# Kernel tuning notes

Hardware: AMD Instinct MI355X
Metric: run time of the kernel (lower is better)

Reference implementation:

```python
import jax, jax.numpy as jnp
import numpy as np

N = 10000
K1, K2 = 10, 25
DIM = 64
OUT = 128
NUM_GRAPHS = 64


def setup_inputs() -> dict:
    key = jax.random.key(0)
    ks = jax.random.split(key, 10)
    h0 = jax.random.normal(ks[0], (N, DIM), jnp.float32)
    h1 = jax.random.normal(ks[1], (N * K1, DIM), jnp.float32)
    h2 = jax.random.normal(ks[2], (N * K1 * K2, DIM), jnp.float32)
    # glorot-ish scaled weights
    w0 = jax.random.normal(ks[3], (2 * DIM, OUT), jnp.float32) * (2.0 / (2 * DIM + OUT)) ** 0.5
    b0 = jnp.zeros((OUT,), jnp.float32)
    w1 = jax.random.normal(ks[4], (2 * OUT, OUT), jnp.float32) * (2.0 / (3 * OUT)) ** 0.5
    b1 = jnp.zeros((OUT,), jnp.float32)
    wr1 = jax.random.normal(ks[5], (OUT, 35), jnp.float32) * (2.0 / (OUT + 35)) ** 0.5
    br1 = jnp.zeros((35,), jnp.float32)
    wr2 = jax.random.normal(ks[6], (35, 35), jnp.float32) * (2.0 / 70) ** 0.5
    br2 = jnp.zeros((35,), jnp.float32)
    wr3 = jax.random.normal(ks[7], (35, 1), jnp.float32) * (2.0 / 36) ** 0.5
    br3 = jnp.zeros((1,), jnp.float32)
    states_graph_ids = jnp.sort(jax.random.randint(ks[8], (N,), 0, NUM_GRAPHS, jnp.int32))
    return {
        "h0": h0, "h1": h1, "h2": h2,
        "w0": w0, "b0": b0, "w1": w1, "b1": b1,
        "wr1": wr1, "br1": br1, "wr2": wr2, "br2": br2, "wr3": wr3, "br3": br3,
        "states_graph_ids": states_graph_ids, "num_graphs": NUM_GRAPHS,
    }


def _aggr_mean(src, neigh, w, b):
    # GraphSAGE mean aggregator: concat(src, mean(neighbors)) @ w + b, relu
    n, d = src.shape
    k = neigh.shape[0] // n
    neigh_mean = neigh.reshape(n, k, d).mean(axis=1)  # (n, d)
    return jax.nn.relu(jnp.concatenate([src, neigh_mean], axis=1) @ w + b)


def reference(h0, h1, h2, w0, b0, w1, b1, wr1, br1, wr2, br2, wr3, br3,
              states_graph_ids, num_graphs):
    # round 0: shared aggregator across depths
    a01 = _aggr_mean(h0, h1, w0, b0)          # (N, OUT)
    a12 = _aggr_mean(h1, h2, w0, b0)          # (N*K1, OUT)
    # round 1
    out = _aggr_mean(a01, a12, w1, b1)        # (N, OUT)
    # segment_sum over sorted graph ids
    seg = jax.ops.segment_sum(out, states_graph_ids, num_segments=num_graphs,
                              indices_are_sorted=True)  # (G, OUT)
    # readout MLP (dropout inactive at inference)
    r = jax.nn.selu(seg @ wr1 + br1)
    r = jax.nn.selu(r @ wr2 + br2)
    r = r @ wr3 + br3                          # (G, 1)
    return r
```

## Files before the change

kernel.cpp:

```cpp
#include <hip/hip_runtime.h>
#include <math.h>

#define N_NODES 10000
#define K1 10
#define K2 25
#define DIM 64
#define OUT 128
#define NGRAPH 64

#define NPB 2
#define RPB (NPB * K1)
#define XROWS (RPB + NPB)
#define QP 36
#define XPITCH (4 * QP)
#define QP1 68
#define X1PITCH (4 * QP1)

__global__ __launch_bounds__(256, 4) void kFused(
    const float* __restrict__ h0, const float* __restrict__ h1,
    const float* __restrict__ h2, const float* __restrict__ w0,
    const float* __restrict__ b0, const float* __restrict__ w1,
    const float* __restrict__ b1, const int* __restrict__ gids,
    float* __restrict__ seg)
{
    __shared__ float xbuf[XROWS][XPITCH];
    __shared__ float x1p[NPB][X1PITCH];

    const int t  = threadIdx.x;
    const int w  = t >> 6;
    const int l  = t & 63;
    const int kq = l & 3;
    const int cp = l >> 2;
    const int c0 = w * 32 + cp * 2;
    const int n0 = blockIdx.x * NPB;

    float w0r0[32], w0r1[32];
#pragma unroll
    for (int kk = 0; kk < 32; ++kk) {
        w0r0[kk] = w0[(kq * 32 + kk) * OUT + c0];
        w0r1[kk] = w0[(kq * 32 + kk) * OUT + c0 + 1];
    }
    const float b00 = b0[c0], b01 = b0[c0 + 1];

    if (t < NPB * DIM) {
        const int i = t >> 6, cl = t & 63;
        xbuf[RPB + i][(cl >> 5) * QP + (cl & 31)] = h0[(size_t)(n0 + i) * DIM + cl];
    }

#pragma unroll 1
    for (int q = 0; q < 5; ++q) {
        const int rloc = w + 4 * q;
        const size_t rg = (size_t)n0 * K1 + rloc;
        const float* hb = h2 + rg * (size_t)(K2 * DIM) + l;
        float s = 0.f;
#pragma unroll
        for (int row = 0; row < K2; ++row)
            s += __builtin_nontemporal_load(hb + row * DIM);
        xbuf[rloc][(2 + (l >> 5)) * QP + (l & 31)] = s * (1.f / K2);
        xbuf[rloc][(l >> 5) * QP + (l & 31)]       = h1[rg * DIM + l];
    }
    __syncthreads();

    if (t < NPB * DIM) {
        const int i = t >> 6, cl = t & 63;
        float s = 0.f;
#pragma unroll
        for (int j = 0; j < K1; ++j)
            s += xbuf[i * K1 + j][(cl >> 5) * QP + (cl & 31)];
        xbuf[RPB + i][(2 + (cl >> 5)) * QP + (cl & 31)] = s * (1.f / K1);
    }
    __syncthreads();

    float accA0 = 0.f, accA1 = 0.f, accB0 = 0.f, accB1 = 0.f;
#pragma unroll 2
    for (int j = 0; j < XROWS; ++j) {
        const float4* xq = (const float4*)&xbuf[j][kq * QP];
        float p0 = 0.f, p1 = 0.f;
#pragma unroll
        for (int m = 0; m < 8; ++m) {
            const float4 x4 = xq[m];
            p0 += x4.x * w0r0[4*m]   + x4.y * w0r0[4*m+1]
                + x4.z * w0r0[4*m+2] + x4.w * w0r0[4*m+3];
            p1 += x4.x * w0r1[4*m]   + x4.y * w0r1[4*m+1]
                + x4.z * w0r1[4*m+2] + x4.w * w0r1[4*m+3];
        }
        p0 += __shfl_xor(p0, 1);  p0 += __shfl_xor(p0, 2);
        p1 += __shfl_xor(p1, 1);  p1 += __shfl_xor(p1, 2);
        const float y0 = fmaxf(p0 + b00, 0.f);
        const float y1 = fmaxf(p1 + b01, 0.f);
        if (j < K1)        { accA0 += y0; accA1 += y1; }
        else if (j < RPB)  { accB0 += y0; accB1 += y1; }
        else if (kq == 0) {
            const int i = j - RPB;
            float2* dst = (float2*)&x1p[i][(c0 >> 6) * QP1 + (c0 & 63)];
            *dst = make_float2(y0, y1);
        }
    }
    if (kq == 0) {
        const int C = OUT + c0;
        float2* d0 = (float2*)&x1p[0][(C >> 6) * QP1 + (C & 63)];
        *d0 = make_float2(accA0 * (1.f / K1), accA1 * (1.f / K1));
        float2* d1 = (float2*)&x1p[1][(C >> 6) * QP1 + (C & 63)];
        *d1 = make_float2(accB0 * (1.f / K1), accB1 * (1.f / K1));
    }
    __syncthreads();

    float pr00 = 0.f, pr01 = 0.f, pr10 = 0.f, pr11 = 0.f;
#pragma unroll 1
    for (int hh = 0; hh < 2; ++hh) {
        float w1r0[32], w1r1[32];
#pragma unroll
        for (int kk = 0; kk < 32; ++kk) {
            const int krow = kq * 64 + hh * 32 + kk;
            w1r0[kk] = w1[krow * OUT + c0];
            w1r1[kk] = w1[krow * OUT + c0 + 1];
        }
        {
            const float4* xq = (const float4*)&x1p[0][kq * QP1 + hh * 32];
            float p0 = 0.f, p1 = 0.f;
#pragma unroll
            for (int m = 0; m < 8; ++m) {
                const float4 x4 = xq[m];
                p0 += x4.x*w1r0[4*m] + x4.y*w1r0[4*m+1] + x4.z*w1r0[4*m+2] + x4.w*w1r0[4*m+3];
                p1 += x4.x*w1r1[4*m] + x4.y*w1r1[4*m+1] + x4.z*w1r1[4*m+2] + x4.w*w1r1[4*m+3];
            }
            pr00 += p0; pr01 += p1;
        }
        {
            const float4* xq = (const float4*)&x1p[1][kq * QP1 + hh * 32];
            float p0 = 0.f, p1 = 0.f;
#pragma unroll
            for (int m = 0; m < 8; ++m) {
                const float4 x4 = xq[m];
                p0 += x4.x*w1r0[4*m] + x4.y*w1r0[4*m+1] + x4.z*w1r0[4*m+2] + x4.w*w1r0[4*m+3];
                p1 += x4.x*w1r1[4*m] + x4.y*w1r1[4*m+1] + x4.z*w1r1[4*m+2] + x4.w*w1r1[4*m+3];
            }
            pr10 += p0; pr11 += p1;
        }
    }
    const float b10 = b1[c0], b11 = b1[c0 + 1];
    pr00 += __shfl_xor(pr00, 1); pr00 += __shfl_xor(pr00, 2);
    pr01 += __shfl_xor(pr01, 1); pr01 += __shfl_xor(pr01, 2);
    pr10 += __shfl_xor(pr10, 1); pr10 += __shfl_xor(pr10, 2);
    pr11 += __shfl_xor(pr11, 1); pr11 += __shfl_xor(pr11, 2);
    const float o00 = fmaxf(pr00 + b10, 0.f);
    const float o01 = fmaxf(pr01 + b11, 0.f);
    const float o10 = fmaxf(pr10 + b10, 0.f);
    const float o11 = fmaxf(pr11 + b11, 0.f);

    if (kq == 0) {
        const int g0 = gids[n0], g1 = gids[n0 + 1];
        if (g0 == g1) {
            atomicAdd(&seg[g0 * OUT + c0],     o00 + o10);
            atomicAdd(&seg[g0 * OUT + c0 + 1], o01 + o11);
        } else {
            atomicAdd(&seg[g0 * OUT + c0],     o00);
            atomicAdd(&seg[g0 * OUT + c0 + 1], o01);
            atomicAdd(&seg[g1 * OUT + c0],     o10);
            atomicAdd(&seg[g1 * OUT + c0 + 1], o11);
        }
    }
}

__global__ void kC(const float* __restrict__ seg,
                   const float* __restrict__ wr1, const float* __restrict__ br1,
                   const float* __restrict__ wr2, const float* __restrict__ br2,
                   const float* __restrict__ wr3, const float* __restrict__ br3,
                   float* __restrict__ out)
{
    __shared__ float r1[35], r2[35];
    const int g = blockIdx.x, l = threadIdx.x;
    const float* s = seg + (size_t)g * OUT;
    const float SCALE = 1.0507009873554805f;
    const float ALPHA = 1.6732632423543772f;

    if (l < 35) {
        float d = br1[l];
        for (int k = 0; k < OUT; ++k) d += s[k] * wr1[k * 35 + l];
        r1[l] = d > 0.f ? SCALE * d : SCALE * ALPHA * (expf(d) - 1.f);
    }
    __syncthreads();
    if (l < 35) {
        float d = br2[l];
        for (int k = 0; k < 35; ++k) d += r1[k] * wr2[k * 35 + l];
        r2[l] = d > 0.f ? SCALE * d : SCALE * ALPHA * (expf(d) - 1.f);
    }
    __syncthreads();
    if (l == 0) {
        float d = br3[0];
        for (int k = 0; k < 35; ++k) d += r2[k] * wr3[k];
        out[g] = d;
    }
}

extern "C" void kernel_launch(void* const* d_in, const int* in_sizes, int n_in,
                              void* d_out, int out_size, void* d_ws, size_t ws_size,
                              hipStream_t stream)
{
    const float* h0  = (const float*)d_in[0];
    const float* h1  = (const float*)d_in[1];
    const float* h2  = (const float*)d_in[2];
    const float* w0  = (const float*)d_in[3];
    const float* b0  = (const float*)d_in[4];
    const float* w1  = (const float*)d_in[5];
    const float* b1  = (const float*)d_in[6];
    const float* wr1 = (const float*)d_in[7];
    const float* br1 = (const float*)d_in[8];
    const float* wr2 = (const float*)d_in[9];
    const float* br2 = (const float*)d_in[10];
    const float* wr3 = (const float*)d_in[11];
    const float* br3 = (const float*)d_in[12];
    const int*  gids = (const int*)d_in[13];

    float* seg = (float*)d_ws;
    float* out = (float*)d_out;

    hipMemsetAsync(seg, 0, NGRAPH * OUT * sizeof(float), stream);
    kFused<<<N_NODES / NPB, 256, 0, stream>>>(h0, h1, h2, w0, b0, w1, b1, gids, seg);
    kC<<<NGRAPH, 64, 0, stream>>>(seg, wr1, br1, wr2, br2, wr3, br3, out);
}
```

Measured before the change: 1.005 ms.

## Restructure fused SAGE kernel with per-column threads, float4 loads and shared-memory k-split

Thread mapping changes from 4-way k-split with shuffle reductions to one output column per thread, with a 2-way k-split whose halves are combined through shared memory. h2 neighbor sums now use float4 loads spread over row groups with cross-lane shuffles, and h1 and h0 are staged with coalesced float4 copies. The w0 load moves after the h2 streaming. Register pressure (64-element weight arrays plus 22 partials) may rise under the 256x4 launch bound, and the non-temporal loads on h2 are dropped.

```diff
diff --git a/kernel.cpp b/kernel.cpp
--- a/kernel.cpp
+++ b/kernel.cpp
@@ -11,10 +11,6 @@
 #define NPB 2
 #define RPB (NPB * K1)
 #define XROWS (RPB + NPB)
-#define QP 36
-#define XPITCH (4 * QP)
-#define QP1 68
-#define X1PITCH (4 * QP1)
 
 __global__ __launch_bounds__(256, 4) void kFused(
     const float* __restrict__ h0, const float* __restrict__ h1,
@@ -23,141 +19,143 @@
     const float* __restrict__ b1, const int* __restrict__ gids,
     float* __restrict__ seg)
 {
-    __shared__ float xbuf[XROWS][XPITCH];
-    __shared__ float x1p[NPB][X1PITCH];
+    __shared__ float xbuf[XROWS][2 * DIM];
+    __shared__ float pbuf[XROWS][OUT];
+    __shared__ float x1[NPB][2 * OUT];
 
     const int t  = threadIdx.x;
     const int w  = t >> 6;
     const int l  = t & 63;
-    const int kq = l & 3;
-    const int cp = l >> 2;
-    const int c0 = w * 32 + cp * 2;
+    const int c  = t & 127;
+    const int h  = t >> 7;
     const int n0 = blockIdx.x * NPB;
 
-    float w0r0[32], w0r1[32];
-#pragma unroll
-    for (int kk = 0; kk < 32; ++kk) {
-        w0r0[kk] = w0[(kq * 32 + kk) * OUT + c0];
-        w0r1[kk] = w0[(kq * 32 + kk) * OUT + c0 + 1];
-    }
-    const float b00 = b0[c0], b01 = b0[c0 + 1];
-
-    if (t < NPB * DIM) {
-        const int i = t >> 6, cl = t & 63;
-        xbuf[RPB + i][(cl >> 5) * QP + (cl & 31)] = h0[(size_t)(n0 + i) * DIM + cl];
-    }
-
+    {
+        const float4* src = (const float4*)(h1 + (size_t)n0 * (K1 * DIM));
+        float4 v = src[t];
+        *(float4*)&xbuf[t >> 4][4 * (t & 15)] = v;
+        if (t < 64) {
+            float4 v2 = src[256 + t];
+            *(float4*)&xbuf[16 + (t >> 4)][4 * (t & 15)] = v2;
+        }
+        if (t < 32) {
+            const float4* s0 = (const float4*)(h0 + (size_t)n0 * DIM);
+            *(float4*)&xbuf[RPB + (t >> 4)][4 * (t & 15)] = s0[t];
+        }
+    }
+
+    {
+        const int fc  = l & 15;
+        const int rg4 = l >> 4;
 #pragma unroll 1
-    for (int q = 0; q < 5; ++q) {
-        const int rloc = w + 4 * q;
-        const size_t rg = (size_t)n0 * K1 + rloc;
-        const float* hb = h2 + rg * (size_t)(K2 * DIM) + l;
-        float s = 0.f;
-#pragma unroll
-        for (int row = 0; row < K2; ++row)
-            s += __builtin_nontemporal_load(hb + row * DIM);
-        xbuf[rloc][(2 + (l >> 5)) * QP + (l & 31)] = s * (1.f / K2);
-        xbuf[rloc][(l >> 5) * QP + (l & 31)]       = h1[rg * DIM + l];
-    }
-    __syncthreads();
+        for (int q = 0; q < 5; ++q) {
+            const int rloc = w + 4 * q;
+            const size_t rg = (size_t)n0 * K1 + rloc;
+            const float4* hb = (const float4*)h2 + rg * (K2 * DIM / 4);
+            float4 s = make_float4(0.f, 0.f, 0.f, 0.f);
+#pragma unroll
+            for (int k = 0; k < 6; ++k) {
+                const float4 v = hb[(4 * k + rg4) * 16 + fc];
+                s.x += v.x; s.y += v.y; s.z += v.z; s.w += v.w;
+            }
+            if (rg4 == 0) {
+                const float4 v = hb[24 * 16 + fc];
+                s.x += v.x; s.y += v.y; s.z += v.z; s.w += v.w;
+            }
+            s.x += __shfl_xor(s.x, 16); s.y += __shfl_xor(s.y, 16);
+            s.z += __shfl_xor(s.z, 16); s.w += __shfl_xor(s.w, 16);
+            s.x += __shfl_xor(s.x, 32); s.y += __shfl_xor(s.y, 32);
+            s.z += __shfl_xor(s.z, 32); s.w += __shfl_xor(s.w, 32);
+            if (rg4 == 0) {
+                *(float4*)&xbuf[rloc][DIM + 4 * fc] =
+                    make_float4(s.x * (1.f / K2), s.y * (1.f / K2),
+                                s.z * (1.f / K2), s.w * (1.f / K2));
+            }
+        }
+    }
+    __syncthreads();
+
+    float w0r[64];
+#pragma unroll
+    for (int k = 0; k < 64; ++k)
+        w0r[k] = w0[(h * 64 + k) * OUT + c];
+    const float b0r = b0[c];
 
     if (t < NPB * DIM) {
         const int i = t >> 6, cl = t & 63;
         float s = 0.f;
 #pragma unroll
         for (int j = 0; j < K1; ++j)
-            s += xbuf[i * K1 + j][(cl >> 5) * QP + (cl & 31)];
-        xbuf[RPB + i][(2 + (cl >> 5)) * QP + (cl & 31)] = s * (1.f / K1);
-    }
-    __syncthreads();
-
-    float accA0 = 0.f, accA1 = 0.f, accB0 = 0.f, accB1 = 0.f;
-#pragma unroll 2
+            s += xbuf[i * K1 + j][cl];
+        xbuf[RPB + i][DIM + cl] = s * (1.f / K1);
+    }
+    __syncthreads();
+
+    float myp[XROWS];
+#pragma unroll
     for (int j = 0; j < XROWS; ++j) {
-        const float4* xq = (const float4*)&xbuf[j][kq * QP];
+        const float4* xj = (const float4*)(&xbuf[j][h * DIM]);
+        float p = 0.f;
+#pragma unroll
+        for (int k4 = 0; k4 < 16; ++k4) {
+            const float4 xv = xj[k4];
+            p += xv.x * w0r[4 * k4 + 0] + xv.y * w0r[4 * k4 + 1]
+               + xv.z * w0r[4 * k4 + 2] + xv.w * w0r[4 * k4 + 3];
+        }
+        if (h == 1) pbuf[j][c] = p;
+        else        myp[j]     = p;
+    }
+    __syncthreads();
+    if (h == 0) {
+        float accA = 0.f, accB = 0.f;
+#pragma unroll
+        for (int j = 0; j < RPB; ++j) {
+            float y = myp[j] + pbuf[j][c] + b0r;
+            y = fmaxf(y, 0.f);
+            if (j < K1) accA += y; else accB += y;
+        }
+        const float y0 = fmaxf(myp[RPB]     + pbuf[RPB][c]     + b0r, 0.f);
+        const float y1 = fmaxf(myp[RPB + 1] + pbuf[RPB + 1][c] + b0r, 0.f);
+        x1[0][c] = y0;
+        x1[1][c] = y1;
+        x1[0][OUT + c] = accA * (1.f / K1);
+        x1[1][OUT + c] = accB * (1.f / K1);
+    }
+    __syncthreads();
+
+    float pr0 = 0.f, pr1 = 0.f;
+#pragma unroll 1
+    for (int half = 0; half < 2; ++half) {
+        float w1r[64];
+#pragma unroll
+        for (int kk = 0; kk < 64; ++kk)
+            w1r[kk] = w1[(h * 128 + half * 64 + kk) * OUT + c];
+        const float4* xa = (const float4*)(&x1[0][h * OUT + half * 64]);
+        const float4* xb = (const float4*)(&x1[1][h * OUT + half * 64]);
         float p0 = 0.f, p1 = 0.f;
 #pragma unroll
-        for (int m = 0; m < 8; ++m) {
-            const float4 x4 = xq[m];
-            p0 += x4.x * w0r0[4*m]   + x4.y * w0r0[4*m+1]
-                + x4.z * w0r0[4*m+2] + x4.w * w0r0[4*m+3];
-            p1 += x4.x * w0r1[4*m]   + x4.y * w0r1[4*m+1]
-                + x4.z * w0r1[4*m+2] + x4.w * w0r1[4*m+3];
-        }
-        p0 += __shfl_xor(p0, 1);  p0 += __shfl_xor(p0, 2);
-        p1 += __shfl_xor(p1, 1);  p1 += __shfl_xor(p1, 2);
-        const float y0 = fmaxf(p0 + b00, 0.f);
-        const float y1 = fmaxf(p1 + b01, 0.f);
-        if (j < K1)        { accA0 += y0; accA1 += y1; }
-        else if (j < RPB)  { accB0 += y0; accB1 += y1; }
-        else if (kq == 0) {
-            const int i = j - RPB;
-            float2* dst = (float2*)&x1p[i][(c0 >> 6) * QP1 + (c0 & 63)];
-            *dst = make_float2(y0, y1);
-        }
-    }
-    if (kq == 0) {
-        const int C = OUT + c0;
-        float2* d0 = (float2*)&x1p[0][(C >> 6) * QP1 + (C & 63)];
-        *d0 = make_float2(accA0 * (1.f / K1), accA1 * (1.f / K1));
-        float2* d1 = (float2*)&x1p[1][(C >> 6) * QP1 + (C & 63)];
-        *d1 = make_float2(accB0 * (1.f / K1), accB1 * (1.f / K1));
-    }
-    __syncthreads();
-
-    float pr00 = 0.f, pr01 = 0.f, pr10 = 0.f, pr11 = 0.f;
-#pragma unroll 1
-    for (int hh = 0; hh < 2; ++hh) {
-        float w1r0[32], w1r1[32];
-#pragma unroll
-        for (int kk = 0; kk < 32; ++kk) {
-            const int krow = kq * 64 + hh * 32 + kk;
-            w1r0[kk] = w1[krow * OUT + c0];
-            w1r1[kk] = w1[krow * OUT + c0 + 1];
-        }
-        {
-            const float4* xq = (const float4*)&x1p[0][kq * QP1 + hh * 32];
-            float p0 = 0.f, p1 = 0.f;
-#pragma unroll
-            for (int m = 0; m < 8; ++m) {
-                const float4 x4 = xq[m];
-                p0 += x4.x*w1r0[4*m] + x4.y*w1r0[4*m+1] + x4.z*w1r0[4*m+2] + x4.w*w1r0[4*m+3];
-                p1 += x4.x*w1r1[4*m] + x4.y*w1r1[4*m+1] + x4.z*w1r1[4*m+2] + x4.w*w1r1[4*m+3];
-            }
-            pr00 += p0; pr01 += p1;
-        }
-        {
-            const float4* xq = (const float4*)&x1p[1][kq * QP1 + hh * 32];
-            float p0 = 0.f, p1 = 0.f;
-#pragma unroll
-            for (int m = 0; m < 8; ++m) {
-                const float4 x4 = xq[m];
-                p0 += x4.x*w1r0[4*m] + x4.y*w1r0[4*m+1] + x4.z*w1r0[4*m+2] + x4.w*w1r0[4*m+3];
-                p1 += x4.x*w1r1[4*m] + x4.y*w1r1[4*m+1] + x4.z*w1r1[4*m+2] + x4.w*w1r1[4*m+3];
-            }
-            pr10 += p0; pr11 += p1;
-        }
-    }
-    const float b10 = b1[c0], b11 = b1[c0 + 1];
-    pr00 += __shfl_xor(pr00, 1); pr00 += __shfl_xor(pr00, 2);
-    pr01 += __shfl_xor(pr01, 1); pr01 += __shfl_xor(pr01, 2);
-    pr10 += __shfl_xor(pr10, 1); pr10 += __shfl_xor(pr10, 2);
-    pr11 += __shfl_xor(pr11, 1); pr11 += __shfl_xor(pr11, 2);
-    const float o00 = fmaxf(pr00 + b10, 0.f);
-    const float o01 = fmaxf(pr01 + b11, 0.f);
-    const float o10 = fmaxf(pr10 + b10, 0.f);
-    const float o11 = fmaxf(pr11 + b11, 0.f);
-
-    if (kq == 0) {
+        for (int k4 = 0; k4 < 16; ++k4) {
+            const float4 a = xa[k4];
+            p0 += a.x * w1r[4 * k4 + 0] + a.y * w1r[4 * k4 + 1]
+                + a.z * w1r[4 * k4 + 2] + a.w * w1r[4 * k4 + 3];
+            const float4 b = xb[k4];
+            p1 += b.x * w1r[4 * k4 + 0] + b.y * w1r[4 * k4 + 1]
+                + b.z * w1r[4 * k4 + 2] + b.w * w1r[4 * k4 + 3];
+        }
+        pr0 += p0; pr1 += p1;
+    }
+    if (h == 1) { pbuf[0][c] = pr0; pbuf[1][c] = pr1; }
+    __syncthreads();
+    if (h == 0) {
+        const float b1r = b1[c];
+        const float o0 = fmaxf(pr0 + pbuf[0][c] + b1r, 0.f);
+        const float o1 = fmaxf(pr1 + pbuf[1][c] + b1r, 0.f);
         const int g0 = gids[n0], g1 = gids[n0 + 1];
         if (g0 == g1) {
-            atomicAdd(&seg[g0 * OUT + c0],     o00 + o10);
-            atomicAdd(&seg[g0 * OUT + c0 + 1], o01 + o11);
+            atomicAdd(&seg[g0 * OUT + c], o0 + o1);
         } else {
-            atomicAdd(&seg[g0 * OUT + c0],     o00);
-            atomicAdd(&seg[g0 * OUT + c0 + 1], o01);
-            atomicAdd(&seg[g1 * OUT + c0],     o10);
-            atomicAdd(&seg[g1 * OUT + c0 + 1], o11);
+            atomicAdd(&seg[g0 * OUT + c], o0);
+            atomicAdd(&seg[g1 * OUT + c], o1);
         }
     }
 }
```

Result: faster. 908.3 us (-9.7%).
